# Optimization experiments

Hardware: AMD Instinct MI355X
Metric: run time of the kernel (lower is better)

Reference implementation:

```python
import jax, jax.numpy as jnp
import numpy as np

N, E, F_IN, H0, H1, H2 = 50000, 800000, 128, 256, 256, 256
NEG = jnp.finfo(jnp.float32).min


def sage_max(x, src, dst, Wl, bl, Wr):
    # PyG SAGEConv(aggr='max'): lin_l(max_j x_j) + lin_r(x_i)
    agg = jax.ops.segment_max(x[src], dst, num_segments=N)  # [N, F]
    agg = jnp.where(agg <= NEG, 0.0, agg)  # isolated nodes -> 0
    return agg @ Wl + bl + x @ Wr


def setup_inputs() -> dict:
    key = jax.random.key(0)
    ks = jax.random.split(key, 16)
    g = lambda k, shp, fan: jax.random.normal(k, shp, jnp.float32) / np.sqrt(fan)
    inp = {
        "x": jax.random.normal(ks[0], (N, F_IN), jnp.float32),
        "edge_index": jax.random.randint(ks[1], (2, E), 0, N, jnp.int64),
        # shared_l1
        "Wl1": g(ks[2], (F_IN, H0), F_IN), "bl1": jnp.zeros((H0,), jnp.float32), "Wr1": g(ks[3], (F_IN, H0), F_IN),
        # shared_l2
        "Wl2": g(ks[4], (H0, H1), H0), "bl2": jnp.zeros((H1,), jnp.float32), "Wr2": g(ks[5], (H0, H1), H0),
        # rtang_l1 + head
        "Wla": g(ks[6], (H1, H2), H1), "bla": jnp.zeros((H2,), jnp.float32), "Wra": g(ks[7], (H1, H2), H1),
        "Wa": g(ks[8], (H2, 1), H2), "ba": jnp.zeros((1,), jnp.float32),
        # movedis_l1 + head
        "Wlm": g(ks[9], (H1, H2), H1), "blm": jnp.zeros((H2,), jnp.float32), "Wrm": g(ks[10], (H1, H2), H1),
        "Wm": g(ks[11], (H2, 1), H2), "bm": jnp.zeros((1,), jnp.float32),
    }
    return inp


def reference(x, edge_index, Wl1, bl1, Wr1, Wl2, bl2, Wr2,
              Wla, bla, Wra, Wa, ba, Wlm, blm, Wrm, Wm, bm):
    src, dst = edge_index[0], edge_index[1]
    h = jax.nn.relu(sage_max(x, src, dst, Wl1, bl1, Wr1))
    h = jax.nn.relu(sage_max(h, src, dst, Wl2, bl2, Wr2))
    rt = jax.nn.relu(sage_max(h, src, dst, Wla, bla, Wra))
    rt = (rt @ Wa + ba).reshape(-1)  # [N]
    mv = jax.nn.relu(sage_max(h, src, dst, Wlm, blm, Wrm))
    mv = (mv @ Wm + bm).reshape(-1)  # [N]
    return (rt, mv)
```

## Files before the change

### kernel.cpp

```cpp
#include <hip/hip_runtime.h>
#include <hip/hip_bf16.h>


#define NN 50000
#define NE 800000
#define HD 256

using bf16 = __hip_bfloat16;
typedef float f32x4 __attribute__((ext_vector_type(4)));
typedef short bf16x8 __attribute__((ext_vector_type(8)));

__device__ __forceinline__ void async16(const void* g, void* l) {
    __builtin_amdgcn_global_load_lds(
        (const __attribute__((address_space(1))) unsigned int*)g,
        (__attribute__((address_space(3))) unsigned int*)l, 16, 0, 0);
}

__device__ __forceinline__ unsigned short f2b(float f) {
    bf16 b = __float2bfloat16(f);
    return __builtin_bit_cast(unsigned short, b);
}

__global__ void k_zero(int* __restrict__ cnt) {
    int i = blockIdx.x * 256 + threadIdx.x;
    if (i < 2 * NN) cnt[i] = 0;
}

__device__ __forceinline__ void pack1(const float* __restrict__ W,
                                      bf16* __restrict__ bt, int idx, int Ktot,
                                      int kofs) {
    int k = idx >> 8, n = idx & 255;
    bt[(size_t)n * Ktot + kofs + k] = __float2bfloat16(W[idx]);
}

#define SC_B 3200
#define EPS 2000
#define GRP 6250
#define PREP_CVT_B 6250
#define PREP_PACK_B 1792
#define PREP_B (SC_B + PREP_CVT_B + PREP_PACK_B)

__global__ void k_prep(const int* __restrict__ ei, int* __restrict__ cnt,
                       unsigned short* __restrict__ srcp,
                       const float* __restrict__ x, bf16* __restrict__ xb,
                       const float* __restrict__ Wl1,
                       const float* __restrict__ Wr1,
                       const float* __restrict__ Wl2,
                       const float* __restrict__ Wr2,
                       const float* __restrict__ Wla,
                       const float* __restrict__ Wra,
                       const float* __restrict__ Wlm,
                       const float* __restrict__ Wrm, bf16* __restrict__ Bt1,
                       bf16* __restrict__ Bt2, bf16* __restrict__ Bta,
                       bf16* __restrict__ Btm) {
    int b = blockIdx.x;
    if (b < SC_B) {
        const int g = b & 7;
        const int s = b >> 3;
        const int base = s * EPS;
        const int glo = g * GRP, ghi = glo + GRP;
#pragma unroll
        for (int i = 0; i < 8; ++i) {
            int e = base + i * 256 + threadIdx.x;
            if (e < base + EPS) {
                int d = ei[NE + e];
                if (d >= glo && d < ghi) {
                    int sub = e & 1;
                    int slot = atomicAdd(&cnt[sub * NN + d], 1);
                    if (slot < 32)
                        srcp[(d << 6) + (sub << 5) + slot] =
                            (unsigned short)ei[e];
                }
            }
        }
    } else if (b < SC_B + PREP_CVT_B) {
        int i = (b - SC_B) * 256 + threadIdx.x;
        float4 v = ((const float4*)x)[i];
        ushort4 o;
        o.x = f2b(v.x); o.y = f2b(v.y); o.z = f2b(v.z); o.w = f2b(v.w);
        ((ushort4*)xb)[i] = o;
    } else {
        int idx = (b - SC_B - PREP_CVT_B) * 256 + threadIdx.x;
        if (idx < 32768) pack1(Wl1, Bt1, idx, 256, 0);
        else if (idx < 65536) pack1(Wr1, Bt1, idx - 32768, 256, 128);
        else if (idx < 131072) pack1(Wl2, Bt2, idx - 65536, 512, 0);
        else if (idx < 196608) pack1(Wr2, Bt2, idx - 131072, 512, 256);
        else if (idx < 262144) pack1(Wla, Bta, idx - 196608, 512, 0);
        else if (idx < 327680) pack1(Wra, Bta, idx - 262144, 512, 256);
        else if (idx < 393216) pack1(Wlm, Btm, idx - 327680, 512, 0);
        else pack1(Wrm, Btm, idx - 393216, 512, 256);
    }
}


__device__ __forceinline__ void amax8(float (&m)[8], uint4 v) {
    m[0] = fmaxf(m[0], __uint_as_float(v.x << 16));
    m[1] = fmaxf(m[1], __uint_as_float(v.x & 0xffff0000u));
    m[2] = fmaxf(m[2], __uint_as_float(v.y << 16));
    m[3] = fmaxf(m[3], __uint_as_float(v.y & 0xffff0000u));
    m[4] = fmaxf(m[4], __uint_as_float(v.z << 16));
    m[5] = fmaxf(m[5], __uint_as_float(v.z & 0xffff0000u));
    m[6] = fmaxf(m[6], __uint_as_float(v.w << 16));
    m[7] = fmaxf(m[7], __uint_as_float(v.w & 0xffff0000u));
}

__device__ __forceinline__ uint4 pack8(const float (&m)[8]) {
    uint4 r;
    r.x = (__float_as_uint(m[0]) >> 16) | (__float_as_uint(m[1]) & 0xffff0000u);
    r.y = (__float_as_uint(m[2]) >> 16) | (__float_as_uint(m[3]) & 0xffff0000u);
    r.z = (__float_as_uint(m[4]) >> 16) | (__float_as_uint(m[5]) & 0xffff0000u);
    r.w = (__float_as_uint(m[6]) >> 16) | (__float_as_uint(m[7]) & 0xffff0000u);
    return r;
}

template <int EPL>
__global__ __launch_bounds__(256) void k_agg(
    const bf16* __restrict__ feat, bf16* __restrict__ agg,
    const int* __restrict__ cnt, const unsigned short* __restrict__ srcp) {
    int node = blockIdx.x * 4 + (threadIdx.x >> 6);
    if (node >= NN) return;
    int lane = threadIdx.x & 63;
    int c0r = cnt[node], c1r = cnt[NN + node];
    const uint4* __restrict__ f4 = (const uint4*)feat;
    float m[8];
#pragma unroll
    for (int i = 0; i < 8; ++i) m[i] = __int_as_float(0xff800000);

    for (int seg = 0; seg < 2; ++seg) {
        const int n = min(seg ? c1r : c0r, 32);
        const unsigned short* __restrict__ lst =
            srcp + (node << 6) + (seg << 5);
        if (EPL == 4) {
            const int half = lane >> 5, sub = lane & 31;
            int e = 0;
            for (; e + 16 <= n; e += 16) {
                int s[8];
#pragma unroll
                for (int j = 0; j < 8; ++j) s[j] = lst[e + 2 * j + half];
                uint4 v[8];
#pragma unroll
                for (int j = 0; j < 8; ++j) v[j] = f4[(size_t)s[j] * 32 + sub];
#pragma unroll
                for (int j = 0; j < 8; ++j) amax8(m, v[j]);
            }
            int rem = n - e;
            if (rem > 8) {
                int s[8];
#pragma unroll
                for (int j = 0; j < 8; ++j) {
                    int ix = e + 2 * j + half;
                    s[j] = lst[ix < n ? ix : n - 1];
                }
                uint4 v[8];
#pragma unroll
                for (int j = 0; j < 8; ++j) v[j] = f4[(size_t)s[j] * 32 + sub];
#pragma unroll
                for (int j = 0; j < 8; ++j) amax8(m, v[j]);
            } else if (rem > 0) {
                int s[4];
#pragma unroll
                for (int j = 0; j < 4; ++j) {
                    int ix = e + 2 * j + half;
                    s[j] = lst[ix < n ? ix : n - 1];
                }
                uint4 v[4];
#pragma unroll
                for (int j = 0; j < 4; ++j) v[j] = f4[(size_t)s[j] * 32 + sub];
#pragma unroll
                for (int j = 0; j < 4; ++j) amax8(m, v[j]);
            }
        } else {
            const int q = lane >> 4, sub = lane & 15;
            int e = 0;
            for (; e + 32 <= n; e += 32) {
                int s[8];
#pragma unroll
                for (int j = 0; j < 8; ++j) s[j] = lst[e + 4 * j + q];
                uint4 v[8];
#pragma unroll
                for (int j = 0; j < 8; ++j) v[j] = f4[(size_t)s[j] * 16 + sub];
#pragma unroll
                for (int j = 0; j < 8; ++j) amax8(m, v[j]);
            }
            int rem = n - e;
            if (rem > 16) {
                int s[8];
#pragma unroll
                for (int j = 0; j < 8; ++j) {
                    int ix = e + 4 * j + q;
                    s[j] = lst[ix < n ? ix : n - 1];
                }
                uint4 v[8];
#pragma unroll
                for (int j = 0; j < 8; ++j) v[j] = f4[(size_t)s[j] * 16 + sub];
#pragma unroll
                for (int j = 0; j < 8; ++j) amax8(m, v[j]);
            } else if (rem > 8) {
                int s[4];
#pragma unroll
                for (int j = 0; j < 4; ++j) {
                    int ix = e + 4 * j + q;
                    s[j] = lst[ix < n ? ix : n - 1];
                }
                uint4 v[4];
#pragma unroll
                for (int j = 0; j < 4; ++j) v[j] = f4[(size_t)s[j] * 16 + sub];
#pragma unroll
                for (int j = 0; j < 4; ++j) amax8(m, v[j]);
            } else if (rem > 4) {
                int s[2];
#pragma unroll
                for (int j = 0; j < 2; ++j) {
                    int ix = e + 4 * j + q;
                    s[j] = lst[ix < n ? ix : n - 1];
                }
                uint4 v[2];
#pragma unroll
                for (int j = 0; j < 2; ++j) v[j] = f4[(size_t)s[j] * 16 + sub];
#pragma unroll
                for (int j = 0; j < 2; ++j) amax8(m, v[j]);
            } else if (rem > 0) {
                int ix = e + q;
                int s = lst[ix < n ? ix : n - 1];
                uint4 v = f4[(size_t)s * 16 + sub];
                amax8(m, v);
            }
        }
    }

    bool nonempty = (c0r + c1r) > 0;
    if (EPL == 4) {
#pragma unroll
        for (int i = 0; i < 8; ++i)
            m[i] = fmaxf(m[i], __shfl_xor(m[i], 32, 64));
        uint4 r = make_uint4(0, 0, 0, 0);
        if (nonempty) r = pack8(m);
        if (lane < 32) ((uint4*)agg)[(size_t)node * 32 + (lane & 31)] = r;
    } else {
#pragma unroll
        for (int i = 0; i < 8; ++i)
            m[i] = fmaxf(m[i], __shfl_xor(m[i], 32, 64));
#pragma unroll
        for (int i = 0; i < 8; ++i)
            m[i] = fmaxf(m[i], __shfl_xor(m[i], 16, 64));
        uint4 r = make_uint4(0, 0, 0, 0);
        if (nonempty) r = pack8(m);
        if (lane < 16) ((uint4*)agg)[(size_t)node * 16 + (lane & 15)] = r;
    }
}

__device__ __forceinline__ void gemm_core256(const bf16* __restrict__ A0,
                                             const bf16* __restrict__ A1, int F,
                                             int Ktot,
                                             const bf16* __restrict__ Bt,
                                             int bm0, int t, short* As,
                                             short* Bs, f32x4 (&acc)[4][8]) {
    const int wave = t >> 6;
    const int lane = t & 63;
    const int q = lane >> 4;
    const int c = lane & 15;
    const int wr = (wave >> 1) * 64;
    const int wcl = (wave & 1) * 128;

    for (int k0 = 0; k0 < Ktot; k0 += 64) {
        const bf16* Asrc = (k0 < F) ? A0 : A1;
        const int kk = (k0 < F) ? k0 : k0 - F;
        __syncthreads();
#pragma unroll
        for (int it = 0; it < 4; ++it) {
            int chunk = it * 256 + t;
            int row = chunk >> 3, kc = chunk & 7;
            int kcg = kc ^ (row & 7);
            int grow = bm0 + row;
            if (grow > NN - 1) grow = NN - 1;
            async16(Asrc + (size_t)grow * F + kk + kcg * 8, &As[chunk * 8]);
        }
#pragma unroll
        for (int it = 0; it < 8; ++it) {
            int chunk = it * 256 + t;
            int row = chunk >> 3, kc = chunk & 7;
            int kcg = kc ^ (row & 7);
            async16(Bt + (size_t)row * Ktot + k0 + kcg * 8, &Bs[chunk * 8]);
        }
        __syncthreads();
#pragma unroll
        for (int ks = 0; ks < 2; ++ks) {
            bf16x8 af[4], bfr[8];
            int ch = (ks * 4 + q) ^ (c & 7);
#pragma unroll
            for (int i = 0; i < 4; ++i)
                af[i] = *(const bf16x8*)&As[(wr + i * 16 + c) * 64 + ch * 8];
#pragma unroll
            for (int j = 0; j < 8; ++j)
                bfr[j] = *(const bf16x8*)&Bs[(wcl + j * 16 + c) * 64 + ch * 8];
#pragma unroll
            for (int i = 0; i < 4; ++i)
#pragma unroll
                for (int j = 0; j < 8; ++j)
                    acc[i][j] = __builtin_amdgcn_mfma_f32_16x16x32_bf16(
                        af[i], bfr[j], acc[i][j], 0, 0, 0);
        }
    }
}

__global__ __launch_bounds__(256, 2) void k_gemm_h(
    const bf16* __restrict__ A0, const bf16* __restrict__ A1, int F, int Ktot,
    const bf16* __restrict__ Bt, const float* __restrict__ bias,
    bf16* __restrict__ Hout) {
    __shared__ __attribute__((aligned(16))) short As[128 * 64];
    __shared__ __attribute__((aligned(16))) short Bs[256 * 64];
    const int t = threadIdx.x;
    const int bm0 = blockIdx.x * 128;
    const int wave = t >> 6;
    const int lane = t & 63;
    const int q = lane >> 4;
    const int c = lane & 15;
    const int wr = (wave >> 1) * 64;
    const int wcl = (wave & 1) * 128;

    f32x4 acc[4][8];
#pragma unroll
    for (int i = 0; i < 4; ++i)
#pragma unroll
        for (int j = 0; j < 8; ++j) acc[i][j] = (f32x4){0.f, 0.f, 0.f, 0.f};
    gemm_core256(A0, A1, F, Ktot, Bt, bm0, t, As, Bs, acc);

    float bcol[8];
#pragma unroll
    for (int j = 0; j < 8; ++j) bcol[j] = bias[wcl + j * 16 + c];
#pragma unroll
    for (int i = 0; i < 4; ++i)
#pragma unroll
        for (int r = 0; r < 4; ++r) {
            int row = bm0 + wr + i * 16 + q * 4 + r;
            if (row < NN) {
#pragma unroll
                for (int j = 0; j < 8; ++j) {
                    int col = wcl + j * 16 + c;
                    float v = fmaxf(acc[i][j][r] + bcol[j], 0.f);
                    Hout[(size_t)row * HD + col] = __float2bfloat16(v);
                }
            }
        }
}

__global__ __launch_bounds__(256, 2) void k_gemm_heads(
    const bf16* __restrict__ A0, const bf16* __restrict__ A1,
    const bf16* __restrict__ Bta, const float* __restrict__ bla,
    const float* __restrict__ Wa, const float* __restrict__ ba,
    const bf16* __restrict__ Btm, const float* __restrict__ blm,
    const float* __restrict__ Wm, const float* __restrict__ bm,
    float* __restrict__ out) {
    __shared__ __attribute__((aligned(16))) short As[128 * 64];
    __shared__ __attribute__((aligned(16))) short Bs[256 * 64];
    const int t = threadIdx.x;
    const int bm0 = blockIdx.x * 128;
    const int z = blockIdx.y;
    const bf16* Bt = z ? Btm : Bta;
    const float* bias = z ? blm : bla;
    const float* Wh = z ? Wm : Wa;
    const float hb = z ? bm[0] : ba[0];
    float* outp = out + (size_t)z * NN;
    const int wave = t >> 6;
    const int lane = t & 63;
    const int q = lane >> 4;
    const int c = lane & 15;
    const int wr = (wave >> 1) * 64;
    const int wcl = (wave & 1) * 128;

    f32x4 acc[4][8];
#pragma unroll
    for (int i = 0; i < 4; ++i)
#pragma unroll
        for (int j = 0; j < 8; ++j) acc[i][j] = (f32x4){0.f, 0.f, 0.f, 0.f};
    gemm_core256(A0, A1, 256, 512, Bt, bm0, t, As, Bs, acc);

    float bcol[8], wcol[8];
#pragma unroll
    for (int j = 0; j < 8; ++j) {
        int col = wcl + j * 16 + c;
        bcol[j] = bias[col];
        wcol[j] = Wh[col];
    }
    float pr[4][4];
#pragma unroll
    for (int i = 0; i < 4; ++i)
#pragma unroll
        for (int r = 0; r < 4; ++r) {
            float p = 0.f;
#pragma unroll
            for (int j = 0; j < 8; ++j)
                p += fmaxf(acc[i][j][r] + bcol[j], 0.f) * wcol[j];
            p += __shfl_xor(p, 1, 64);
            p += __shfl_xor(p, 2, 64);
            p += __shfl_xor(p, 4, 64);
            p += __shfl_xor(p, 8, 64);
            pr[i][r] = p;
        }
    __syncthreads();
    float* red = (float*)As;
    if ((wave & 1) && c == 0) {
#pragma unroll
        for (int i = 0; i < 4; ++i)
#pragma unroll
            for (int r = 0; r < 4; ++r) red[wr + i * 16 + q * 4 + r] = pr[i][r];
    }
    __syncthreads();
    if (!(wave & 1) && c == 0) {
#pragma unroll
        for (int i = 0; i < 4; ++i)
#pragma unroll
            for (int r = 0; r < 4; ++r) {
                int lr = wr + i * 16 + q * 4 + r;
                int row = bm0 + lr;
                if (row < NN) outp[row] = pr[i][r] + red[lr] + hb;
            }
    }
}

extern "C" void kernel_launch(void* const* d_in, const int* in_sizes, int n_in,
                              void* d_out, int out_size, void* d_ws,
                              size_t ws_size, hipStream_t stream) {
    const float* x = (const float*)d_in[0];
    const int* ei = (const int*)d_in[1];
    const float* Wl1 = (const float*)d_in[2];
    const float* bl1 = (const float*)d_in[3];
    const float* Wr1 = (const float*)d_in[4];
    const float* Wl2 = (const float*)d_in[5];
    const float* bl2 = (const float*)d_in[6];
    const float* Wr2 = (const float*)d_in[7];
    const float* Wla = (const float*)d_in[8];
    const float* bla = (const float*)d_in[9];
    const float* Wra = (const float*)d_in[10];
    const float* Wa = (const float*)d_in[11];
    const float* ba = (const float*)d_in[12];
    const float* Wlm = (const float*)d_in[13];
    const float* blm = (const float*)d_in[14];
    const float* Wrm = (const float*)d_in[15];
    const float* Wm = (const float*)d_in[16];
    const float* bm = (const float*)d_in[17];
    float* out = (float*)d_out;

    char* ws = (char*)d_ws;
    size_t off = 0;
    auto alloc = [&](size_t b) {
        void* p = ws + off;
        off = (off + b + 255) & ~(size_t)255;
        return p;
    };
    unsigned short* srcp = (unsigned short*)alloc((size_t)NN * 64 * 2);
    int* cnt = (int*)alloc((size_t)2 * NN * 4);
    bf16* xb = (bf16*)alloc((size_t)NN * 128 * 2);
    bf16* h1 = (bf16*)alloc((size_t)NN * 256 * 2);
    bf16* h2 = (bf16*)alloc((size_t)NN * 256 * 2);
    bf16* agg = (bf16*)alloc((size_t)NN * 256 * 2);
    bf16* Bt1 = (bf16*)alloc((size_t)256 * 256 * 2);
    bf16* Bt2 = (bf16*)alloc((size_t)256 * 512 * 2);
    bf16* Bta = (bf16*)alloc((size_t)256 * 512 * 2);
    bf16* Btm = (bf16*)alloc((size_t)256 * 512 * 2);
    (void)ws_size; (void)in_sizes; (void)n_in; (void)out_size;

    k_zero<<<(2 * NN + 255) / 256, 256, 0, stream>>>(cnt);
    k_prep<<<PREP_B, 256, 0, stream>>>(ei, cnt, srcp, x, xb, Wl1, Wr1, Wl2,
                                       Wr2, Wla, Wra, Wlm, Wrm, Bt1, Bt2, Bta,
                                       Btm);

    const int GB = (NN + 127) / 128;
    const int NG4 = (NN + 3) / 4;
    k_agg<2><<<NG4, 256, 0, stream>>>(xb, agg, cnt, srcp);
    k_gemm_h<<<GB, 256, 0, stream>>>(agg, xb, 128, 256, Bt1, bl1, h1);
    k_agg<4><<<NG4, 256, 0, stream>>>(h1, agg, cnt, srcp);
    k_gemm_h<<<GB, 256, 0, stream>>>(agg, h1, 256, 512, Bt2, bl2, h2);
    k_agg<4><<<NG4, 256, 0, stream>>>(h2, agg, cnt, srcp);
    dim3 gh(GB, 2);
    k_gemm_heads<<<gh, 256, 0, stream>>>(agg, h2, Bta, bla, Wa, ba, Btm, blm,
                                         Wm, bm, out);
}
```

Baseline: 352.2 us.

## Merge both head GEMMs into one 512-thread block sharing the A tile

```diff
diff --git a/kernel.cpp b/kernel.cpp
--- a/kernel.cpp
+++ b/kernel.cpp
@@ -344,7 +344,7 @@
         }
 }
 
-__global__ __launch_bounds__(256, 2) void k_gemm_heads(
+__global__ __launch_bounds__(512, 2) void k_gemm_heads(
     const bf16* __restrict__ A0, const bf16* __restrict__ A1,
     const bf16* __restrict__ Bta, const float* __restrict__ bla,
     const float* __restrict__ Wa, const float* __restrict__ ba,
@@ -352,33 +352,76 @@
     const float* __restrict__ Wm, const float* __restrict__ bm,
     float* __restrict__ out) {
     __shared__ __attribute__((aligned(16))) short As[128 * 64];
-    __shared__ __attribute__((aligned(16))) short Bs[256 * 64];
+    __shared__ __attribute__((aligned(16))) short Bs[512 * 64];
     const int t = threadIdx.x;
     const int bm0 = blockIdx.x * 128;
-    const int z = blockIdx.y;
-    const bf16* Bt = z ? Btm : Bta;
+    const int wave = t >> 6;
+    const int lane = t & 63;
+    const int q = lane >> 4;
+    const int c = lane & 15;
+    const int wr = (wave >> 2) * 64;
+    const int cg = wave & 3;
+    const int z = cg >> 1;
+    const int wcl = cg * 128;
+    const int Ktot = 512, F = 256;
+
+    f32x4 acc[4][8];
+#pragma unroll
+    for (int i = 0; i < 4; ++i)
+#pragma unroll
+        for (int j = 0; j < 8; ++j) acc[i][j] = (f32x4){0.f, 0.f, 0.f, 0.f};
+
+    for (int k0 = 0; k0 < Ktot; k0 += 64) {
+        const bf16* Asrc = (k0 < F) ? A0 : A1;
+        const int kk = (k0 < F) ? k0 : k0 - F;
+        __syncthreads();
+#pragma unroll
+        for (int it = 0; it < 2; ++it) {
+            int chunk = it * 512 + t;
+            int row = chunk >> 3, kc = chunk & 7;
+            int kcg = kc ^ (row & 7);
+            int grow = bm0 + row;
+            if (grow > NN - 1) grow = NN - 1;
+            async16(Asrc + (size_t)grow * F + kk + kcg * 8, &As[chunk * 8]);
+        }
+#pragma unroll
+        for (int it = 0; it < 8; ++it) {
+            int chunk = it * 512 + t;
+            int row = chunk >> 3, kc = chunk & 7;
+            int kcg = kc ^ (row & 7);
+            const bf16* B = (row < 256) ? Bta : Btm;
+            int brow = row & 255;
+            async16(B + (size_t)brow * Ktot + k0 + kcg * 8, &Bs[chunk * 8]);
+        }
+        __syncthreads();
+#pragma unroll
+        for (int ks = 0; ks < 2; ++ks) {
+            bf16x8 af[4], bfr[8];
+            int ch = (ks * 4 + q) ^ (c & 15 & 7);
+#pragma unroll
+            for (int i = 0; i < 4; ++i)
+                af[i] = *(const bf16x8*)&As[(wr + i * 16 + c) * 64 + ch * 8];
+#pragma unroll
+            for (int j = 0; j < 8; ++j)
+                bfr[j] = *(const bf16x8*)&Bs[(wcl + j * 16 + c) * 64 + ch * 8];
+#pragma unroll
+            for (int i = 0; i < 4; ++i)
+#pragma unroll
+                for (int j = 0; j < 8; ++j)
+                    acc[i][j] = __builtin_amdgcn_mfma_f32_16x16x32_bf16(
+                        af[i], bfr[j], acc[i][j], 0, 0, 0);
+        }
+    }
+
     const float* bias = z ? blm : bla;
     const float* Wh = z ? Wm : Wa;
     const float hb = z ? bm[0] : ba[0];
     float* outp = out + (size_t)z * NN;
-    const int wave = t >> 6;
-    const int lane = t & 63;
-    const int q = lane >> 4;
-    const int c = lane & 15;
-    const int wr = (wave >> 1) * 64;
-    const int wcl = (wave & 1) * 128;
-
-    f32x4 acc[4][8];
-#pragma unroll
-    for (int i = 0; i < 4; ++i)
-#pragma unroll
-        for (int j = 0; j < 8; ++j) acc[i][j] = (f32x4){0.f, 0.f, 0.f, 0.f};
-    gemm_core256(A0, A1, 256, 512, Bt, bm0, t, As, Bs, acc);
-
+    const int colbase = (cg & 1) * 128;
     float bcol[8], wcol[8];
 #pragma unroll
     for (int j = 0; j < 8; ++j) {
-        int col = wcl + j * 16 + c;
+        int col = colbase + j * 16 + c;
         bcol[j] = bias[col];
         wcol[j] = Wh[col];
     }
@@ -399,11 +442,13 @@
         }
     __syncthreads();
     float* red = (float*)As;
+    const int region = wave >> 1;
     if ((wave & 1) && c == 0) {
 #pragma unroll
         for (int i = 0; i < 4; ++i)
 #pragma unroll
-            for (int r = 0; r < 4; ++r) red[wr + i * 16 + q * 4 + r] = pr[i][r];
+            for (int r = 0; r < 4; ++r)
+                red[region * 64 + i * 16 + q * 4 + r] = pr[i][r];
     }
     __syncthreads();
     if (!(wave & 1) && c == 0) {
@@ -411,9 +456,10 @@
         for (int i = 0; i < 4; ++i)
 #pragma unroll
             for (int r = 0; r < 4; ++r) {
-                int lr = wr + i * 16 + q * 4 + r;
-                int row = bm0 + lr;
-                if (row < NN) outp[row] = pr[i][r] + red[lr] + hb;
+                int lr = i * 16 + q * 4 + r;
+                int row = bm0 + wr + lr;
+                if (row < NN)
+                    outp[row] = pr[i][r] + red[region * 64 + lr] + hb;
             }
     }
 }
@@ -472,7 +518,6 @@
     k_agg<4><<<NG4, 256, 0, stream>>>(h1, agg, cnt, srcp);
     k_gemm_h<<<GB, 256, 0, stream>>>(agg, h1, 256, 512, Bt2, bl2, h2);
     k_agg<4><<<NG4, 256, 0, stream>>>(h2, agg, cnt, srcp);
-    dim3 gh(GB, 2);
-    k_gemm_heads<<<gh, 256, 0, stream>>>(agg, h2, Bta, bla, Wa, ba, Btm, blm,
+    k_gemm_heads<<<GB, 512, 0, stream>>>(agg, h2, Bta, bla, Wa, ba, Btm, blm,
                                          Wm, bm, out);
 }
```

New measurement: 359.8 us. 2.2% more time.
